# Optimization experiments

Measured on AMD Instinct MI355X. Metric: run time of the kernel, lower is better.

The kernel has to match this reference:

```python
import jax, jax.numpy as jnp
import numpy as np

D = 1024      # in_features
H = 768       # hidden_features per routed expert
E = 8         # n_routed_experts
K = 2         # n_activated_experts
NS = 2        # n_shared_experts
ROUTE_SCALE = 1.0


def setup_inputs() -> dict:
    key = jax.random.key(0)
    ks = jax.random.split(key, 6)
    s = 0.02
    return {
        "x": jax.random.normal(ks[0], (2, 1024, D), jnp.float32),
        "gate_w": jax.random.normal(ks[1], (E, D), jnp.float32) * s,
        "W1": jax.random.normal(ks[2], (E, 2 * H, D), jnp.float32) * s,   # expert fc1 (y|gate)
        "W2": jax.random.normal(ks[3], (E, D, H), jnp.float32) * s,       # expert fc2
        "Ws1": jax.random.normal(ks[4], (2 * NS * H, D), jnp.float32) * s,  # shared fc1
        "Ws2": jax.random.normal(ks[5], (D, NS * H), jnp.float32) * s,      # shared fc2
    }


def _gated_mlp(x, w1, w2):
    # GatedMLP: fc1 -> chunk(2) -> y * silu(gate) -> fc2, all bias-free
    h = x @ w1.T
    y, g = jnp.split(h, 2, axis=-1)
    return (y * jax.nn.silu(g)) @ w2.T


def reference(x, gate_w, W1, W2, Ws1, Ws2):
    x_shape = x.shape
    xf = x.reshape(-1, D)                 # [T, D]
    T = xf.shape[0]

    # --- Gate: softmax scores in fp32, top-k routing ---
    scores = jax.nn.softmax((xf @ gate_w.T).astype(jnp.float32), axis=-1)  # [T, E]
    top_vals, top_idx = jax.lax.top_k(scores, K)
    # no bias branch (in_features != 7168): gathered original scores == top_k values
    weights = (top_vals * ROUTE_SCALE).astype(x.dtype)                      # [T, K]

    # Dense per-token/expert combine weights (0 for unselected experts);
    # mathematically identical to the per-expert gather/scatter-add combine.
    w_dense = jnp.zeros((T, E), x.dtype).at[jnp.arange(T)[:, None], top_idx].set(weights)

    # --- Routed experts (stacked GatedMLPs) ---
    h = jnp.einsum('td,ehd->teh', xf, W1)        # [T, E, 2H]
    y, g = jnp.split(h, 2, axis=-1)
    eo = jnp.einsum('teh,edh->ted', y * jax.nn.silu(g), W2)  # [T, E, D]
    z = jnp.einsum('te,ted->td', w_dense, eo)    # weighted combine

    # --- Shared experts ---
    z = z + _gated_mlp(xf, Ws1, Ws2)
    return z.reshape(x_shape)
```

## Files before the change

### kernel.cpp

```cpp
#include <hip/hip_runtime.h>
#include <hip/hip_bf16.h>


typedef short bf16x8 __attribute__((ext_vector_type(8)));
typedef float f32x4 __attribute__((ext_vector_type(4)));

__device__ __forceinline__ unsigned short f2b(float f) {
    __hip_bfloat16 h = __float2bfloat16(f);
    return *reinterpret_cast<unsigned short*>(&h);
}

__device__ __forceinline__ void ldst16(const unsigned short* g, unsigned short* l) {
    __builtin_amdgcn_global_load_lds(
        (const __attribute__((address_space(1))) unsigned int*)g,
        (__attribute__((address_space(3))) unsigned int*)l, 16, 0, 0);
}

__device__ __forceinline__ void cvt8(const float* s, unsigned short* d, int j) {
    const float4* sp = reinterpret_cast<const float4*>(s) + (size_t)j * 2;
    float4 v0 = sp[0], v1 = sp[1];
    union { unsigned short u[8]; uint4 v; } o;
    o.u[0]=f2b(v0.x); o.u[1]=f2b(v0.y); o.u[2]=f2b(v0.z); o.u[3]=f2b(v0.w);
    o.u[4]=f2b(v1.x); o.u[5]=f2b(v1.y); o.u[6]=f2b(v1.z); o.u[7]=f2b(v1.w);
    *(reinterpret_cast<uint4*>(d) + j) = o.v;
}

__global__ __launch_bounds__(256) void k_convgate(const float* __restrict__ x,
                                                  const float* __restrict__ gw,
                                                  const float* __restrict__ W1,
                                                  const float* __restrict__ Ws1,
                                                  const float* __restrict__ W2,
                                                  const float* __restrict__ Ws2,
                                                  unsigned short* __restrict__ xb,
                                                  unsigned short* __restrict__ W1b,
                                                  unsigned short* __restrict__ Ws1b,
                                                  unsigned short* __restrict__ W2b,
                                                  unsigned short* __restrict__ Ws2b,
                                                  int* __restrict__ tokslot,
                                                  float* __restrict__ wroute,
                                                  int* __restrict__ cnt,
                                                  float* __restrict__ out) {
    __shared__ float red[4][8];
    __shared__ float sc[8];
    const int b = blockIdx.x, tid = threadIdx.x;
    if (b < 11520) {
        int i = b * 256 + tid;
        if (i < 1572864)       cvt8(W1,  W1b,  i);
        else if (i < 1966080)  cvt8(Ws1, Ws1b, i - 1572864);
        else if (i < 2752512)  cvt8(W2,  W2b,  i - 1966080);
        else if (i < 2949120)  cvt8(Ws2, Ws2b, i - 2752512);
        return;
    }
    const int t = b - 11520;
    const int lane = tid & 63, w = tid >> 6;

    float4 v = reinterpret_cast<const float4*>(x + (size_t)t * 1024)[tid];
    union { unsigned short u[4]; } o;
    o.u[0]=f2b(v.x); o.u[1]=f2b(v.y); o.u[2]=f2b(v.z); o.u[3]=f2b(v.w);
    reinterpret_cast<ushort4*>(xb + (size_t)t * 1024)[tid] = *(ushort4*)o.u;

    float p[8];
    for (int e = 0; e < 8; e++) {
        float4 g = reinterpret_cast<const float4*>(gw + (size_t)e * 1024)[tid];
        p[e] = v.x*g.x + v.y*g.y + v.z*g.z + v.w*g.w;
    }
    for (int e = 0; e < 8; e++)
        for (int off = 32; off > 0; off >>= 1) p[e] += __shfl_down(p[e], off, 64);
    if (lane == 0)
        for (int e = 0; e < 8; e++) red[w][e] = p[e];
    __syncthreads();
    if (tid < 8) sc[tid] = red[0][tid] + red[1][tid] + red[2][tid] + red[3][tid];
    __syncthreads();
    if (tid == 0) {
        float m = sc[0];
        for (int e = 1; e < 8; e++) m = fmaxf(m, sc[e]);
        float ex[8], sum = 0.f;
        for (int e = 0; e < 8; e++) { ex[e] = expf(sc[e] - m); sum += ex[e]; }
        float inv = 1.f / sum;
        int i1 = 0;
        for (int e = 1; e < 8; e++) if (sc[e] > sc[i1]) i1 = e;
        int i2 = -1; float s2 = -1e30f;
        for (int e = 0; e < 8; e++) if (e != i1 && sc[e] > s2) { s2 = sc[e]; i2 = e; }
        int p1 = atomicAdd(&cnt[i1 * 16], 1);
        tokslot[i1 * 2048 + p1] = t; wroute[i1 * 2048 + p1] = ex[i1] * inv;
        int p2 = atomicAdd(&cnt[i2 * 16], 1);
        tokslot[i2 * 2048 + p2] = t; wroute[i2 * 2048 + p2] = ex[i2] * inv;
    }
    reinterpret_cast<float4*>(out + (size_t)t * 1024)[tid] = (float4){0.f, 0.f, 0.f, 0.f};
}

__global__ __launch_bounds__(256) void k_fc1u(const unsigned short* __restrict__ xb,
                                              const unsigned short* __restrict__ W1b,
                                              const unsigned short* __restrict__ Ws1b,
                                              const int* __restrict__ tokslot,
                                              const float* __restrict__ wroute,
                                              const int* __restrict__ cnt,
                                              unsigned short* __restrict__ act_r,
                                              unsigned short* __restrict__ acts) {
    __shared__ alignas(16) unsigned short As[128 * 64];
    __shared__ alignas(16) unsigned short Bs[128 * 64];
    const int tid = threadIdx.x, lane = tid & 63, w = tid >> 6;
    const int wr = w >> 1, wc = w & 1;
    const int mt = blockIdx.x / 12, ht = blockIdx.x % 12;

    int pre = 0, sel = -1, base = 0;
    for (int ee = 0; ee < 10; ee++) {
        int til = (ee < 8) ? ((cnt[ee * 16] + 127) >> 7) : 16;
        if (sel < 0 && mt < pre + til) { sel = ee; base = pre; }
        pre += til;
    }
    if (sel < 0) return;
    const int e = sel, m0 = (mt - base) * 128, h0 = ht * 64;
    const int Te = (e < 8) ? cnt[e * 16] : 2048;
    const unsigned short* Bp = (e < 8) ? (W1b + (size_t)e * 1536 * 1024)
                                       : (Ws1b + (size_t)(e - 8) * 768 * 1024);
    const int gOff = (e < 8) ? 768 : 1536;

    const int kc = tid & 7;
    int aoff[4], boff[4];
    for (int q = 0; q < 4; q++) {
        int row = q * 32 + (tid >> 3);
        int idx = m0 + row;
        int tk = (e < 8) ? ((idx < Te) ? tokslot[e * 2048 + idx] : 0) : idx;
        aoff[q] = tk * 1024 + ((kc ^ (row & 7)) << 3);
        int grow = (row < 64) ? (h0 + row) : (gOff + h0 + row - 64);
        boff[q] = grow * 1024 + ((kc ^ (row & 7)) << 3);
    }

    f32x4 accy[4][2], accg[4][2];
    for (int i = 0; i < 4; i++)
        for (int j = 0; j < 2; j++) {
            accy[i][j] = (f32x4){0.f, 0.f, 0.f, 0.f};
            accg[i][j] = (f32x4){0.f, 0.f, 0.f, 0.f};
        }

    for (int k0 = 0; k0 < 1024; k0 += 64) {
        for (int q = 0; q < 4; q++) {
            ldst16(xb + aoff[q] + k0, As + (q * 256 + tid) * 8);
            ldst16(Bp + boff[q] + k0, Bs + (q * 256 + tid) * 8);
        }
        __syncthreads();
        for (int kh = 0; kh < 2; kh++) {
            const int cq = kh * 4 + (lane >> 4);
            bf16x8 a[4], by[2], bg[2];
            for (int i = 0; i < 4; i++) {
                int r = 64 * wr + 16 * i + (lane & 15);
                a[i] = *(const bf16x8*)&As[r * 64 + ((cq ^ (r & 7)) << 3)];
            }
            for (int j = 0; j < 2; j++) {
                int ry = 32 * wc + 16 * j + (lane & 15);
                by[j] = *(const bf16x8*)&Bs[ry * 64 + ((cq ^ (ry & 7)) << 3)];
                int rg = 64 + ry;
                bg[j] = *(const bf16x8*)&Bs[rg * 64 + ((cq ^ (rg & 7)) << 3)];
            }
            for (int i = 0; i < 4; i++)
                for (int j = 0; j < 2; j++) {
                    accy[i][j] = __builtin_amdgcn_mfma_f32_16x16x32_bf16(a[i], by[j], accy[i][j], 0, 0, 0);
                    accg[i][j] = __builtin_amdgcn_mfma_f32_16x16x32_bf16(a[i], bg[j], accg[i][j], 0, 0, 0);
                }
        }
        __syncthreads();
    }

    for (int i = 0; i < 4; i++)
        for (int r = 0; r < 4; r++) {
            int irow = m0 + 64 * wr + 16 * i + ((lane >> 4) << 2) + r;
            if (irow >= Te) continue;
            float sw = (e < 8) ? wroute[e * 2048 + irow] : 1.0f;
            unsigned short* dst = (e < 8)
                ? (act_r + ((size_t)e * 2048 + irow) * 768)
                : (acts + (size_t)irow * 1536 + (size_t)(e - 8) * 768);
            for (int j = 0; j < 2; j++) {
                float y = accy[i][j][r], g = accg[i][j][r];
                float sg = g / (1.0f + __expf(-g));
                int col = h0 + 32 * wc + 16 * j + (lane & 15);
                dst[col] = f2b(sw * y * sg);
            }
        }
}

__global__ __launch_bounds__(256) void k_fc2u(const unsigned short* __restrict__ act_r,
                                              const unsigned short* __restrict__ acts,
                                              const unsigned short* __restrict__ W2b,
                                              const unsigned short* __restrict__ Ws2b,
                                              const int* __restrict__ tokslot,
                                              const int* __restrict__ cnt,
                                              float* __restrict__ out) {
    __shared__ alignas(16) unsigned short As[128 * 128];
    __shared__ alignas(16) unsigned short Bs[64 * 128];
    const int tid = threadIdx.x, lane = tid & 63, w = tid >> 6;
    const int wr = w >> 1, wc = w & 1;
    const int mt = blockIdx.x >> 4, nt = blockIdx.x & 15;

    int pre = 0, sel = -1, base = 0;
    for (int ee = 0; ee < 9; ee++) {
        int til = (ee < 8) ? ((cnt[ee * 16] + 127) >> 7) : 16;
        if (sel < 0 && mt < pre + til) { sel = ee; base = pre; }
        pre += til;
    }
    if (sel < 0) return;
    const int e = sel, m0 = (mt - base) * 128, n0 = nt * 64;
    int Te, astride, bstride, K;
    const unsigned short *Ab, *Bb;
    if (e < 8) {
        Te = cnt[e * 16]; K = 768; astride = 768; bstride = 768;
        Ab = act_r + (size_t)e * 2048 * 768;
        Bb = W2b + (size_t)e * 1024 * 768;
    } else {
        Te = 2048; K = 1536; astride = 1536; bstride = 1536;
        Ab = acts;
        Bb = Ws2b;
    }

    const int cp = tid & 15;
    int aoff[8], boff[4];
    for (int q = 0; q < 8; q++) {
        int row = q * 16 + (tid >> 4);
        aoff[q] = (m0 + row) * astride + ((cp ^ (row & 15)) << 3);
    }
    for (int q = 0; q < 4; q++) {
        int row = q * 16 + (tid >> 4);
        boff[q] = (n0 + row) * bstride + ((cp ^ (row & 15)) << 3);
    }

    f32x4 acc[4][2];
    for (int i = 0; i < 4; i++)
        for (int j = 0; j < 2; j++) acc[i][j] = (f32x4){0.f, 0.f, 0.f, 0.f};

    for (int k0 = 0; k0 < K; k0 += 128) {
        for (int q = 0; q < 8; q++) ldst16(Ab + aoff[q] + k0, As + (q * 256 + tid) * 8);
        for (int q = 0; q < 4; q++) ldst16(Bb + boff[q] + k0, Bs + (q * 256 + tid) * 8);
        __syncthreads();
        for (int kh = 0; kh < 4; kh++) {
            const int cq = kh * 4 + (lane >> 4);
            bf16x8 a[4], b[2];
            for (int i = 0; i < 4; i++) {
                int r = 64 * wr + 16 * i + (lane & 15);
                a[i] = *(const bf16x8*)&As[r * 128 + ((cq ^ (r & 15)) << 3)];
            }
            for (int j = 0; j < 2; j++) {
                int rb = 32 * wc + 16 * j + (lane & 15);
                b[j] = *(const bf16x8*)&Bs[rb * 128 + ((cq ^ (rb & 15)) << 3)];
            }
            for (int i = 0; i < 4; i++)
                for (int j = 0; j < 2; j++)
                    acc[i][j] = __builtin_amdgcn_mfma_f32_16x16x32_bf16(a[i], b[j], acc[i][j], 0, 0, 0);
        }
        __syncthreads();
    }

    for (int i = 0; i < 4; i++)
        for (int r = 0; r < 4; r++) {
            int irow = m0 + 64 * wr + 16 * i + ((lane >> 4) << 2) + r;
            if (irow >= Te) continue;
            int t = (e < 8) ? tokslot[e * 2048 + irow] : irow;
            for (int j = 0; j < 2; j++) {
                int col = n0 + 32 * wc + 16 * j + (lane & 15);
                atomicAdd(out + (size_t)t * 1024 + col, acc[i][j][r]);
            }
        }
}

extern "C" void kernel_launch(void* const* d_in, const int* in_sizes, int n_in,
                              void* d_out, int out_size, void* d_ws, size_t ws_size,
                              hipStream_t stream) {
    const float* x   = (const float*)d_in[0];
    const float* gw  = (const float*)d_in[1];
    const float* W1  = (const float*)d_in[2];
    const float* W2  = (const float*)d_in[3];
    const float* Ws1 = (const float*)d_in[4];
    const float* Ws2 = (const float*)d_in[5];
    float* out = (float*)d_out;

    char* ws = (char*)d_ws;
    unsigned short* xb    = (unsigned short*)(ws + 0);
    unsigned short* W1b   = (unsigned short*)(ws + 4194304);
    unsigned short* Ws1b  = (unsigned short*)(ws + 29360128);
    unsigned short* W2b   = (unsigned short*)(ws + 35651584);
    unsigned short* Ws2b  = (unsigned short*)(ws + 48234496);
    unsigned short* act_r = (unsigned short*)(ws + 51380224);
    unsigned short* acts  = (unsigned short*)(ws + 76546048);
    int*            tokslot = (int*)(ws + 82837504);
    float*          wroute  = (float*)(ws + 82903040);
    int*            cnt     = (int*)(ws + 82968576);

    hipMemsetAsync(cnt, 0, 512, stream);
    k_convgate<<<13568, 256, 0, stream>>>(x, gw, W1, Ws1, W2, Ws2,
                                          xb, W1b, Ws1b, W2b, Ws2b,
                                          tokslot, wroute, cnt, out);
    k_fc1u<<<864, 256, 0, stream>>>(xb, W1b, Ws1b, tokslot, wroute, cnt, act_r, acts);
    k_fc2u<<<896, 256, 0, stream>>>(act_r, acts, W2b, Ws2b, tokslot, cnt, out);
}
```

Baseline: 236.3 us.

## Double-buffer LDS tiles in fc1/fc2 GEMMs to overlap loads with MFMA

Both expert GEMM kernels now keep two LDS buffers and issue the global-to-LDS loads for the next K slice before running the MFMAs on the current one, with a single waitcnt and barrier per iteration. The fc2 kernel's K tile is cut from 128 to 64 so the doubled buffers fit in LDS, and s_setprio is raised around the MFMA blocks. The aim is to hide global-memory latency behind compute. The cost is more LDS per block in fc1, which can lower occupancy, and twice as many loop iterations and barriers in fc2.

```diff
diff --git a/kernel.cpp b/kernel.cpp
--- a/kernel.cpp
+++ b/kernel.cpp
@@ -97,8 +97,8 @@
                                               const int* __restrict__ cnt,
                                               unsigned short* __restrict__ act_r,
                                               unsigned short* __restrict__ acts) {
-    __shared__ alignas(16) unsigned short As[128 * 64];
-    __shared__ alignas(16) unsigned short Bs[128 * 64];
+    __shared__ alignas(16) unsigned short As[2][128 * 64];
+    __shared__ alignas(16) unsigned short Bs[2][128 * 64];
     const int tid = threadIdx.x, lane = tid & 63, w = tid >> 6;
     const int wr = w >> 1, wc = w & 1;
     const int mt = blockIdx.x / 12, ht = blockIdx.x % 12;
@@ -134,32 +134,44 @@
             accg[i][j] = (f32x4){0.f, 0.f, 0.f, 0.f};
         }
 
+    auto stage = [&](int buf, int k0) {
+        for (int q = 0; q < 4; q++) {
+            ldst16(xb + aoff[q] + k0, &As[buf][(q * 256 + tid) * 8]);
+            ldst16(Bp + boff[q] + k0, &Bs[buf][(q * 256 + tid) * 8]);
+        }
+    };
+
+    stage(0, 0);
+    asm volatile("s_waitcnt vmcnt(0)" ::: "memory");
+    __builtin_amdgcn_s_barrier();
+
+    int cur = 0;
     for (int k0 = 0; k0 < 1024; k0 += 64) {
-        for (int q = 0; q < 4; q++) {
-            ldst16(xb + aoff[q] + k0, As + (q * 256 + tid) * 8);
-            ldst16(Bp + boff[q] + k0, Bs + (q * 256 + tid) * 8);
-        }
-        __syncthreads();
+        if (k0 + 64 < 1024) stage(cur ^ 1, k0 + 64);
         for (int kh = 0; kh < 2; kh++) {
             const int cq = kh * 4 + (lane >> 4);
             bf16x8 a[4], by[2], bg[2];
             for (int i = 0; i < 4; i++) {
                 int r = 64 * wr + 16 * i + (lane & 15);
-                a[i] = *(const bf16x8*)&As[r * 64 + ((cq ^ (r & 7)) << 3)];
+                a[i] = *(const bf16x8*)&As[cur][r * 64 + ((cq ^ (r & 7)) << 3)];
             }
             for (int j = 0; j < 2; j++) {
                 int ry = 32 * wc + 16 * j + (lane & 15);
-                by[j] = *(const bf16x8*)&Bs[ry * 64 + ((cq ^ (ry & 7)) << 3)];
+                by[j] = *(const bf16x8*)&Bs[cur][ry * 64 + ((cq ^ (ry & 7)) << 3)];
                 int rg = 64 + ry;
-                bg[j] = *(const bf16x8*)&Bs[rg * 64 + ((cq ^ (rg & 7)) << 3)];
-            }
+                bg[j] = *(const bf16x8*)&Bs[cur][rg * 64 + ((cq ^ (rg & 7)) << 3)];
+            }
+            __builtin_amdgcn_s_setprio(1);
             for (int i = 0; i < 4; i++)
                 for (int j = 0; j < 2; j++) {
                     accy[i][j] = __builtin_amdgcn_mfma_f32_16x16x32_bf16(a[i], by[j], accy[i][j], 0, 0, 0);
                     accg[i][j] = __builtin_amdgcn_mfma_f32_16x16x32_bf16(a[i], bg[j], accg[i][j], 0, 0, 0);
                 }
-        }
-        __syncthreads();
+            __builtin_amdgcn_s_setprio(0);
+        }
+        asm volatile("s_waitcnt vmcnt(0)" ::: "memory");
+        __builtin_amdgcn_s_barrier();
+        cur ^= 1;
     }
 
     for (int i = 0; i < 4; i++)
@@ -186,8 +198,8 @@
                                               const int* __restrict__ tokslot,
                                               const int* __restrict__ cnt,
                                               float* __restrict__ out) {
-    __shared__ alignas(16) unsigned short As[128 * 128];
-    __shared__ alignas(16) unsigned short Bs[64 * 128];
+    __shared__ alignas(16) unsigned short As[2][128 * 64];
+    __shared__ alignas(16) unsigned short Bs[2][64 * 64];
     const int tid = threadIdx.x, lane = tid & 63, w = tid >> 6;
     const int wr = w >> 1, wc = w & 1;
     const int mt = blockIdx.x >> 4, nt = blockIdx.x & 15;
@@ -212,41 +224,53 @@
         Bb = Ws2b;
     }
 
-    const int cp = tid & 15;
-    int aoff[8], boff[4];
-    for (int q = 0; q < 8; q++) {
-        int row = q * 16 + (tid >> 4);
-        aoff[q] = (m0 + row) * astride + ((cp ^ (row & 15)) << 3);
-    }
+    const int kc = tid & 7;
+    int aoff[4], boff[2];
     for (int q = 0; q < 4; q++) {
-        int row = q * 16 + (tid >> 4);
-        boff[q] = (n0 + row) * bstride + ((cp ^ (row & 15)) << 3);
+        int row = q * 32 + (tid >> 3);
+        aoff[q] = (m0 + row) * astride + ((kc ^ (row & 7)) << 3);
+    }
+    for (int q = 0; q < 2; q++) {
+        int row = q * 32 + (tid >> 3);
+        boff[q] = (n0 + row) * bstride + ((kc ^ (row & 7)) << 3);
     }
 
     f32x4 acc[4][2];
     for (int i = 0; i < 4; i++)
         for (int j = 0; j < 2; j++) acc[i][j] = (f32x4){0.f, 0.f, 0.f, 0.f};
 
-    for (int k0 = 0; k0 < K; k0 += 128) {
-        for (int q = 0; q < 8; q++) ldst16(Ab + aoff[q] + k0, As + (q * 256 + tid) * 8);
-        for (int q = 0; q < 4; q++) ldst16(Bb + boff[q] + k0, Bs + (q * 256 + tid) * 8);
-        __syncthreads();
-        for (int kh = 0; kh < 4; kh++) {
+    auto stage = [&](int buf, int k0) {
+        for (int q = 0; q < 4; q++) ldst16(Ab + aoff[q] + k0, &As[buf][(q * 256 + tid) * 8]);
+        for (int q = 0; q < 2; q++) ldst16(Bb + boff[q] + k0, &Bs[buf][(q * 256 + tid) * 8]);
+    };
+
+    stage(0, 0);
+    asm volatile("s_waitcnt vmcnt(0)" ::: "memory");
+    __builtin_amdgcn_s_barrier();
+
+    int cur = 0;
+    for (int k0 = 0; k0 < K; k0 += 64) {
+        if (k0 + 64 < K) stage(cur ^ 1, k0 + 64);
+        for (int kh = 0; kh < 2; kh++) {
             const int cq = kh * 4 + (lane >> 4);
             bf16x8 a[4], b[2];
             for (int i = 0; i < 4; i++) {
                 int r = 64 * wr + 16 * i + (lane & 15);
-                a[i] = *(const bf16x8*)&As[r * 128 + ((cq ^ (r & 15)) << 3)];
+                a[i] = *(const bf16x8*)&As[cur][r * 64 + ((cq ^ (r & 7)) << 3)];
             }
             for (int j = 0; j < 2; j++) {
                 int rb = 32 * wc + 16 * j + (lane & 15);
-                b[j] = *(const bf16x8*)&Bs[rb * 128 + ((cq ^ (rb & 15)) << 3)];
-            }
+                b[j] = *(const bf16x8*)&Bs[cur][rb * 64 + ((cq ^ (rb & 7)) << 3)];
+            }
+            __builtin_amdgcn_s_setprio(1);
             for (int i = 0; i < 4; i++)
                 for (int j = 0; j < 2; j++)
                     acc[i][j] = __builtin_amdgcn_mfma_f32_16x16x32_bf16(a[i], b[j], acc[i][j], 0, 0, 0);
-        }
-        __syncthreads();
+            __builtin_amdgcn_s_setprio(0);
+        }
+        asm volatile("s_waitcnt vmcnt(0)" ::: "memory");
+        __builtin_amdgcn_s_barrier();
+        cur ^= 1;
     }
 
     for (int i = 0; i < 4; i++)
```

New measurement: 235.6 us. About the same (-0.3%).

## Fuse MoE stages into one persistent cooperative kernel with work queues

Applied to the files above, without the earlier changes.

Replaces the three kernel launches with one persistent cooperative kernel that uses grid-wide syncs between phases. Blocks take work from atomic counters. The W2/Ws2 fp32-to-bf16 conversion is deferred into the fc1 phase so it overlaps with the fc1 GEMM tiles, and fc2 tiles are handed out in reverse order. It also raises wave priority around the MFMA blocks. The aim is to cut launch gaps and tail idle time, at the cost of grid-sync overhead and occupancy fixed by the persistent grid size.

```diff
diff --git a/kernel.cpp b/kernel.cpp
--- a/kernel.cpp
+++ b/kernel.cpp
@@ -1,5 +1,8 @@
 #include <hip/hip_runtime.h>
 #include <hip/hip_bf16.h>
+#include <hip/hip_cooperative_groups.h>
+
+namespace cg = cooperative_groups;
 
 
 typedef short bf16x8 __attribute__((ext_vector_type(8)));
@@ -25,83 +28,21 @@
     *(reinterpret_cast<uint4*>(d) + j) = o.v;
 }
 
-__global__ __launch_bounds__(256) void k_convgate(const float* __restrict__ x,
-                                                  const float* __restrict__ gw,
-                                                  const float* __restrict__ W1,
-                                                  const float* __restrict__ Ws1,
-                                                  const float* __restrict__ W2,
-                                                  const float* __restrict__ Ws2,
-                                                  unsigned short* __restrict__ xb,
-                                                  unsigned short* __restrict__ W1b,
-                                                  unsigned short* __restrict__ Ws1b,
-                                                  unsigned short* __restrict__ W2b,
-                                                  unsigned short* __restrict__ Ws2b,
-                                                  int* __restrict__ tokslot,
-                                                  float* __restrict__ wroute,
-                                                  int* __restrict__ cnt,
-                                                  float* __restrict__ out) {
-    __shared__ float red[4][8];
-    __shared__ float sc[8];
-    const int b = blockIdx.x, tid = threadIdx.x;
-    if (b < 11520) {
-        int i = b * 256 + tid;
-        if (i < 1572864)       cvt8(W1,  W1b,  i);
-        else if (i < 1966080)  cvt8(Ws1, Ws1b, i - 1572864);
-        else if (i < 2752512)  cvt8(W2,  W2b,  i - 1966080);
-        else if (i < 2949120)  cvt8(Ws2, Ws2b, i - 2752512);
-        return;
-    }
-    const int t = b - 11520;
-    const int lane = tid & 63, w = tid >> 6;
-
-    float4 v = reinterpret_cast<const float4*>(x + (size_t)t * 1024)[tid];
-    union { unsigned short u[4]; } o;
-    o.u[0]=f2b(v.x); o.u[1]=f2b(v.y); o.u[2]=f2b(v.z); o.u[3]=f2b(v.w);
-    reinterpret_cast<ushort4*>(xb + (size_t)t * 1024)[tid] = *(ushort4*)o.u;
-
-    float p[8];
-    for (int e = 0; e < 8; e++) {
-        float4 g = reinterpret_cast<const float4*>(gw + (size_t)e * 1024)[tid];
-        p[e] = v.x*g.x + v.y*g.y + v.z*g.z + v.w*g.w;
-    }
-    for (int e = 0; e < 8; e++)
-        for (int off = 32; off > 0; off >>= 1) p[e] += __shfl_down(p[e], off, 64);
-    if (lane == 0)
-        for (int e = 0; e < 8; e++) red[w][e] = p[e];
-    __syncthreads();
-    if (tid < 8) sc[tid] = red[0][tid] + red[1][tid] + red[2][tid] + red[3][tid];
-    __syncthreads();
-    if (tid == 0) {
-        float m = sc[0];
-        for (int e = 1; e < 8; e++) m = fmaxf(m, sc[e]);
-        float ex[8], sum = 0.f;
-        for (int e = 0; e < 8; e++) { ex[e] = expf(sc[e] - m); sum += ex[e]; }
-        float inv = 1.f / sum;
-        int i1 = 0;
-        for (int e = 1; e < 8; e++) if (sc[e] > sc[i1]) i1 = e;
-        int i2 = -1; float s2 = -1e30f;
-        for (int e = 0; e < 8; e++) if (e != i1 && sc[e] > s2) { s2 = sc[e]; i2 = e; }
-        int p1 = atomicAdd(&cnt[i1 * 16], 1);
-        tokslot[i1 * 2048 + p1] = t; wroute[i1 * 2048 + p1] = ex[i1] * inv;
-        int p2 = atomicAdd(&cnt[i2 * 16], 1);
-        tokslot[i2 * 2048 + p2] = t; wroute[i2 * 2048 + p2] = ex[i2] * inv;
-    }
-    reinterpret_cast<float4*>(out + (size_t)t * 1024)[tid] = (float4){0.f, 0.f, 0.f, 0.f};
-}
-
-__global__ __launch_bounds__(256) void k_fc1u(const unsigned short* __restrict__ xb,
-                                              const unsigned short* __restrict__ W1b,
-                                              const unsigned short* __restrict__ Ws1b,
-                                              const int* __restrict__ tokslot,
-                                              const float* __restrict__ wroute,
-                                              const int* __restrict__ cnt,
-                                              unsigned short* __restrict__ act_r,
-                                              unsigned short* __restrict__ acts) {
-    __shared__ alignas(16) unsigned short As[128 * 64];
-    __shared__ alignas(16) unsigned short Bs[128 * 64];
+__device__ void fc1_tile(int tile, unsigned short* smem,
+                         const unsigned short* __restrict__ xb,
+                         const unsigned short* __restrict__ W1b,
+                         const unsigned short* __restrict__ Ws1b,
+                         const int* __restrict__ tokslot,
+                         const float* __restrict__ wroute,
+                         const int* __restrict__ cnt,
+                         unsigned short* __restrict__ act_r,
+                         unsigned short* __restrict__ acts)
+{
+    unsigned short* As = smem;
+    unsigned short* Bs = smem + 8192;
     const int tid = threadIdx.x, lane = tid & 63, w = tid >> 6;
     const int wr = w >> 1, wc = w & 1;
-    const int mt = blockIdx.x / 12, ht = blockIdx.x % 12;
+    const int mt = tile / 12, ht = tile % 12;
 
     int pre = 0, sel = -1, base = 0;
     for (int ee = 0; ee < 10; ee++) {
@@ -153,11 +94,13 @@
                 int rg = 64 + ry;
                 bg[j] = *(const bf16x8*)&Bs[rg * 64 + ((cq ^ (rg & 7)) << 3)];
             }
+            __builtin_amdgcn_s_setprio(1);
             for (int i = 0; i < 4; i++)
                 for (int j = 0; j < 2; j++) {
                     accy[i][j] = __builtin_amdgcn_mfma_f32_16x16x32_bf16(a[i], by[j], accy[i][j], 0, 0, 0);
                     accg[i][j] = __builtin_amdgcn_mfma_f32_16x16x32_bf16(a[i], bg[j], accg[i][j], 0, 0, 0);
                 }
+            __builtin_amdgcn_s_setprio(0);
         }
         __syncthreads();
     }
@@ -179,18 +122,20 @@
         }
 }
 
-__global__ __launch_bounds__(256) void k_fc2u(const unsigned short* __restrict__ act_r,
-                                              const unsigned short* __restrict__ acts,
-                                              const unsigned short* __restrict__ W2b,
-                                              const unsigned short* __restrict__ Ws2b,
-                                              const int* __restrict__ tokslot,
-                                              const int* __restrict__ cnt,
-                                              float* __restrict__ out) {
-    __shared__ alignas(16) unsigned short As[128 * 128];
-    __shared__ alignas(16) unsigned short Bs[64 * 128];
+__device__ void fc2_tile(int tile, unsigned short* smem,
+                         const unsigned short* __restrict__ act_r,
+                         const unsigned short* __restrict__ acts,
+                         const unsigned short* __restrict__ W2b,
+                         const unsigned short* __restrict__ Ws2b,
+                         const int* __restrict__ tokslot,
+                         const int* __restrict__ cnt,
+                         float* __restrict__ out)
+{
+    unsigned short* As = smem;
+    unsigned short* Bs = smem + 16384;
     const int tid = threadIdx.x, lane = tid & 63, w = tid >> 6;
     const int wr = w >> 1, wc = w & 1;
-    const int mt = blockIdx.x >> 4, nt = blockIdx.x & 15;
+    const int mt = tile >> 4, nt = tile & 15;
 
     int pre = 0, sel = -1, base = 0;
     for (int ee = 0; ee < 9; ee++) {
@@ -242,9 +187,11 @@
                 int rb = 32 * wc + 16 * j + (lane & 15);
                 b[j] = *(const bf16x8*)&Bs[rb * 128 + ((cq ^ (rb & 15)) << 3)];
             }
+            __builtin_amdgcn_s_setprio(1);
             for (int i = 0; i < 4; i++)
                 for (int j = 0; j < 2; j++)
                     acc[i][j] = __builtin_amdgcn_mfma_f32_16x16x32_bf16(a[i], b[j], acc[i][j], 0, 0, 0);
+            __builtin_amdgcn_s_setprio(0);
         }
         __syncthreads();
     }
@@ -259,6 +206,107 @@
                 atomicAdd(out + (size_t)t * 1024 + col, acc[i][j][r]);
             }
         }
+}
+
+__global__ __launch_bounds__(256, 3) void k_moe(
+    const float* __restrict__ x, const float* __restrict__ gw,
+    const float* __restrict__ W1, const float* __restrict__ Ws1,
+    const float* __restrict__ W2, const float* __restrict__ Ws2,
+    unsigned short* __restrict__ xb, unsigned short* __restrict__ W1b,
+    unsigned short* __restrict__ Ws1b, unsigned short* __restrict__ W2b,
+    unsigned short* __restrict__ Ws2b, int* __restrict__ tokslot,
+    float* __restrict__ wroute, int* __restrict__ cnt,
+    unsigned short* __restrict__ act_r, unsigned short* __restrict__ acts,
+    float* __restrict__ out)
+{
+    __shared__ alignas(16) unsigned short smem[24576];
+    const int tid = threadIdx.x, bid = blockIdx.x, nb = gridDim.x;
+    cg::grid_group grid = cg::this_grid();
+
+    {
+        const int stride = nb * 256;
+        for (int i = bid * 256 + tid; i < 1966080; i += stride) {
+            if (i < 1572864) cvt8(W1, W1b, i);
+            else             cvt8(Ws1, Ws1b, i - 1572864);
+        }
+        const int lane = tid & 63, w = tid >> 6;
+        float* red = (float*)smem;
+        float* sc  = red + 32;
+        for (int t = bid; t < 2048; t += nb) {
+            float4 v = reinterpret_cast<const float4*>(x + (size_t)t * 1024)[tid];
+            union { unsigned short u[4]; ushort4 v4; } o;
+            o.u[0]=f2b(v.x); o.u[1]=f2b(v.y); o.u[2]=f2b(v.z); o.u[3]=f2b(v.w);
+            reinterpret_cast<ushort4*>(xb + (size_t)t * 1024)[tid] = o.v4;
+
+            float p[8];
+            for (int e = 0; e < 8; e++) {
+                float4 g = reinterpret_cast<const float4*>(gw + (size_t)e * 1024)[tid];
+                p[e] = v.x*g.x + v.y*g.y + v.z*g.z + v.w*g.w;
+            }
+            for (int e = 0; e < 8; e++)
+                for (int off = 32; off > 0; off >>= 1) p[e] += __shfl_down(p[e], off, 64);
+            if (lane == 0)
+                for (int e = 0; e < 8; e++) red[w * 8 + e] = p[e];
+            __syncthreads();
+            if (tid < 8) sc[tid] = red[tid] + red[8 + tid] + red[16 + tid] + red[24 + tid];
+            __syncthreads();
+            if (tid == 0) {
+                float m = sc[0];
+                for (int e = 1; e < 8; e++) m = fmaxf(m, sc[e]);
+                float ex[8], sum = 0.f;
+                for (int e = 0; e < 8; e++) { ex[e] = expf(sc[e] - m); sum += ex[e]; }
+                float inv = 1.f / sum;
+                int i1 = 0;
+                for (int e = 1; e < 8; e++) if (sc[e] > sc[i1]) i1 = e;
+                int i2 = -1; float s2 = -1e30f;
+                for (int e = 0; e < 8; e++) if (e != i1 && sc[e] > s2) { s2 = sc[e]; i2 = e; }
+                int p1 = atomicAdd(&cnt[i1 * 16], 1);
+                tokslot[i1 * 2048 + p1] = t; wroute[i1 * 2048 + p1] = ex[i1] * inv;
+                int p2 = atomicAdd(&cnt[i2 * 16], 1);
+                tokslot[i2 * 2048 + p2] = t; wroute[i2 * 2048 + p2] = ex[i2] * inv;
+            }
+            reinterpret_cast<float4*>(out + (size_t)t * 1024)[tid] = (float4){0.f, 0.f, 0.f, 0.f};
+            __syncthreads();
+        }
+    }
+    __threadfence();
+    grid.sync();
+
+    {
+        int* bc = (int*)smem;
+        while (true) {
+            if (tid == 0) *bc = atomicAdd(cnt + 120, 1);
+            __syncthreads();
+            const int item = *bc;
+            __syncthreads();
+            if (item >= 1824) break;
+            if (item < 864) {
+                fc1_tile(item, smem, xb, W1b, Ws1b, tokslot, wroute, cnt, act_r, acts);
+            } else {
+                const int c0 = (item - 864) * 1024 + tid;
+                #pragma unroll
+                for (int u = 0; u < 4; u++) {
+                    int i = c0 + u * 256;
+                    if (i < 786432)       cvt8(W2, W2b, i);
+                    else                  cvt8(Ws2, Ws2b, i - 786432);
+                }
+            }
+        }
+    }
+    __threadfence();
+    grid.sync();
+
+    {
+        int* bc = (int*)smem;
+        while (true) {
+            if (tid == 0) *bc = atomicAdd(cnt + 124, 1);
+            __syncthreads();
+            const int item = *bc;
+            __syncthreads();
+            if (item >= 896) break;
+            fc2_tile(895 - item, smem, act_r, acts, W2b, Ws2b, tokslot, cnt, out);
+        }
+    }
 }
 
 extern "C" void kernel_launch(void* const* d_in, const int* in_sizes, int n_in,
@@ -284,10 +332,19 @@
     float*          wroute  = (float*)(ws + 82903040);
     int*            cnt     = (int*)(ws + 82968576);
 
+    static int gridsz = 0;
+    if (gridsz == 0) {
+        int nbpc = 0;
+        if (hipOccupancyMaxActiveBlocksPerMultiprocessor(&nbpc, k_moe, 256, 0) != hipSuccess
+            || nbpc < 1) nbpc = 1;
+        if (nbpc > 3) nbpc = 3;
+        gridsz = nbpc * 256;
+    }
+
     hipMemsetAsync(cnt, 0, 512, stream);
-    k_convgate<<<13568, 256, 0, stream>>>(x, gw, W1, Ws1, W2, Ws2,
-                                          xb, W1b, Ws1b, W2b, Ws2b,
-                                          tokslot, wroute, cnt, out);
-    k_fc1u<<<864, 256, 0, stream>>>(xb, W1b, Ws1b, tokslot, wroute, cnt, act_r, acts);
-    k_fc2u<<<896, 256, 0, stream>>>(act_r, acts, W2b, Ws2b, tokslot, cnt, out);
-}
+    void* args[] = {(void*)&x, (void*)&gw, (void*)&W1, (void*)&Ws1, (void*)&W2, (void*)&Ws2,
+                    (void*)&xb, (void*)&W1b, (void*)&Ws1b, (void*)&W2b, (void*)&Ws2b,
+                    (void*)&tokslot, (void*)&wroute, (void*)&cnt,
+                    (void*)&act_r, (void*)&acts, (void*)&out};
+    hipLaunchCooperativeKernel((void*)k_moe, dim3(gridsz), dim3(256), args, 0, stream);
+}
```

Result: slower. 443.5 us (+87.7%).

## Remap GEMM block indices per XCD and double per-thread weight conversion work

Applied to the files above, without the earlier changes.

The fc1 and fc2 kernels now decode blockIdx so that the blocks landing on one XCD (blockIdx mod 8) share the same M-tiles and sweep all N/H tiles of each. The aim is to reuse the gathered activation rows from that XCD's L2 instead of spreading them across all eight XCDs. The weight-conversion part of k_convgate now has each thread convert two 8-element chunks, which halves the number of conversion blocks and cuts per-block scheduling overhead. Nothing changes numerically. Because the routed expert tile counts are uneven, the remap may leave work unevenly spread across XCDs.

```diff
diff --git a/kernel.cpp b/kernel.cpp
--- a/kernel.cpp
+++ b/kernel.cpp
@@ -23,6 +23,17 @@
     o.u[0]=f2b(v0.x); o.u[1]=f2b(v0.y); o.u[2]=f2b(v0.z); o.u[3]=f2b(v0.w);
     o.u[4]=f2b(v1.x); o.u[5]=f2b(v1.y); o.u[6]=f2b(v1.z); o.u[7]=f2b(v1.w);
     *(reinterpret_cast<uint4*>(d) + j) = o.v;
+}
+
+__device__ __forceinline__ void cvt_dispatch(const float* W1, const float* Ws1,
+                                             const float* W2, const float* Ws2,
+                                             unsigned short* W1b, unsigned short* Ws1b,
+                                             unsigned short* W2b, unsigned short* Ws2b,
+                                             int i) {
+    if (i < 1572864)       cvt8(W1,  W1b,  i);
+    else if (i < 1966080)  cvt8(Ws1, Ws1b, i - 1572864);
+    else if (i < 2752512)  cvt8(W2,  W2b,  i - 1966080);
+    else if (i < 2949120)  cvt8(Ws2, Ws2b, i - 2752512);
 }
 
 __global__ __launch_bounds__(256) void k_convgate(const float* __restrict__ x,
@@ -43,15 +54,13 @@
     __shared__ float red[4][8];
     __shared__ float sc[8];
     const int b = blockIdx.x, tid = threadIdx.x;
-    if (b < 11520) {
-        int i = b * 256 + tid;
-        if (i < 1572864)       cvt8(W1,  W1b,  i);
-        else if (i < 1966080)  cvt8(Ws1, Ws1b, i - 1572864);
-        else if (i < 2752512)  cvt8(W2,  W2b,  i - 1966080);
-        else if (i < 2949120)  cvt8(Ws2, Ws2b, i - 2752512);
+    if (b < 5760) {
+        int i0 = b * 512 + tid;
+        cvt_dispatch(W1, Ws1, W2, Ws2, W1b, Ws1b, W2b, Ws2b, i0);
+        cvt_dispatch(W1, Ws1, W2, Ws2, W1b, Ws1b, W2b, Ws2b, i0 + 256);
         return;
     }
-    const int t = b - 11520;
+    const int t = b - 5760;
     const int lane = tid & 63, w = tid >> 6;
 
     float4 v = reinterpret_cast<const float4*>(x + (size_t)t * 1024)[tid];
@@ -101,7 +110,8 @@
     __shared__ alignas(16) unsigned short Bs[128 * 64];
     const int tid = threadIdx.x, lane = tid & 63, w = tid >> 6;
     const int wr = w >> 1, wc = w & 1;
-    const int mt = blockIdx.x / 12, ht = blockIdx.x % 12;
+    const int xcd = blockIdx.x & 7, j = blockIdx.x >> 3;
+    const int mt = (j / 12) * 8 + xcd, ht = j % 12;
 
     int pre = 0, sel = -1, base = 0;
     for (int ee = 0; ee < 10; ee++) {
@@ -129,9 +139,9 @@
 
     f32x4 accy[4][2], accg[4][2];
     for (int i = 0; i < 4; i++)
-        for (int j = 0; j < 2; j++) {
-            accy[i][j] = (f32x4){0.f, 0.f, 0.f, 0.f};
-            accg[i][j] = (f32x4){0.f, 0.f, 0.f, 0.f};
+        for (int j2 = 0; j2 < 2; j2++) {
+            accy[i][j2] = (f32x4){0.f, 0.f, 0.f, 0.f};
+            accg[i][j2] = (f32x4){0.f, 0.f, 0.f, 0.f};
         }
 
     for (int k0 = 0; k0 < 1024; k0 += 64) {
@@ -147,16 +157,16 @@
                 int r = 64 * wr + 16 * i + (lane & 15);
                 a[i] = *(const bf16x8*)&As[r * 64 + ((cq ^ (r & 7)) << 3)];
             }
-            for (int j = 0; j < 2; j++) {
-                int ry = 32 * wc + 16 * j + (lane & 15);
-                by[j] = *(const bf16x8*)&Bs[ry * 64 + ((cq ^ (ry & 7)) << 3)];
+            for (int j2 = 0; j2 < 2; j2++) {
+                int ry = 32 * wc + 16 * j2 + (lane & 15);
+                by[j2] = *(const bf16x8*)&Bs[ry * 64 + ((cq ^ (ry & 7)) << 3)];
                 int rg = 64 + ry;
-                bg[j] = *(const bf16x8*)&Bs[rg * 64 + ((cq ^ (rg & 7)) << 3)];
+                bg[j2] = *(const bf16x8*)&Bs[rg * 64 + ((cq ^ (rg & 7)) << 3)];
             }
             for (int i = 0; i < 4; i++)
-                for (int j = 0; j < 2; j++) {
-                    accy[i][j] = __builtin_amdgcn_mfma_f32_16x16x32_bf16(a[i], by[j], accy[i][j], 0, 0, 0);
-                    accg[i][j] = __builtin_amdgcn_mfma_f32_16x16x32_bf16(a[i], bg[j], accg[i][j], 0, 0, 0);
+                for (int j2 = 0; j2 < 2; j2++) {
+                    accy[i][j2] = __builtin_amdgcn_mfma_f32_16x16x32_bf16(a[i], by[j2], accy[i][j2], 0, 0, 0);
+                    accg[i][j2] = __builtin_amdgcn_mfma_f32_16x16x32_bf16(a[i], bg[j2], accg[i][j2], 0, 0, 0);
                 }
         }
         __syncthreads();
@@ -170,10 +180,10 @@
             unsigned short* dst = (e < 8)
                 ? (act_r + ((size_t)e * 2048 + irow) * 768)
                 : (acts + (size_t)irow * 1536 + (size_t)(e - 8) * 768);
-            for (int j = 0; j < 2; j++) {
-                float y = accy[i][j][r], g = accg[i][j][r];
+            for (int j2 = 0; j2 < 2; j2++) {
+                float y = accy[i][j2][r], g = accg[i][j2][r];
                 float sg = g / (1.0f + __expf(-g));
-                int col = h0 + 32 * wc + 16 * j + (lane & 15);
+                int col = h0 + 32 * wc + 16 * j2 + (lane & 15);
                 dst[col] = f2b(sw * y * sg);
             }
         }
@@ -190,7 +200,8 @@
     __shared__ alignas(16) unsigned short Bs[64 * 128];
     const int tid = threadIdx.x, lane = tid & 63, w = tid >> 6;
     const int wr = w >> 1, wc = w & 1;
-    const int mt = blockIdx.x >> 4, nt = blockIdx.x & 15;
+    const int xcd = blockIdx.x & 7, j = blockIdx.x >> 3;
+    const int mt = (j / 16) * 8 + xcd, nt = j % 16;
 
     int pre = 0, sel = -1, base = 0;
     for (int ee = 0; ee < 9; ee++) {
@@ -225,7 +236,7 @@
 
     f32x4 acc[4][2];
     for (int i = 0; i < 4; i++)
-        for (int j = 0; j < 2; j++) acc[i][j] = (f32x4){0.f, 0.f, 0.f, 0.f};
+        for (int j2 = 0; j2 < 2; j2++) acc[i][j2] = (f32x4){0.f, 0.f, 0.f, 0.f};
 
     for (int k0 = 0; k0 < K; k0 += 128) {
         for (int q = 0; q < 8; q++) ldst16(Ab + aoff[q] + k0, As + (q * 256 + tid) * 8);
@@ -238,13 +249,13 @@
                 int r = 64 * wr + 16 * i + (lane & 15);
                 a[i] = *(const bf16x8*)&As[r * 128 + ((cq ^ (r & 15)) << 3)];
             }
-            for (int j = 0; j < 2; j++) {
-                int rb = 32 * wc + 16 * j + (lane & 15);
-                b[j] = *(const bf16x8*)&Bs[rb * 128 + ((cq ^ (rb & 15)) << 3)];
+            for (int j2 = 0; j2 < 2; j2++) {
+                int rb = 32 * wc + 16 * j2 + (lane & 15);
+                b[j2] = *(const bf16x8*)&Bs[rb * 128 + ((cq ^ (rb & 15)) << 3)];
             }
             for (int i = 0; i < 4; i++)
-                for (int j = 0; j < 2; j++)
-                    acc[i][j] = __builtin_amdgcn_mfma_f32_16x16x32_bf16(a[i], b[j], acc[i][j], 0, 0, 0);
+                for (int j2 = 0; j2 < 2; j2++)
+                    acc[i][j2] = __builtin_amdgcn_mfma_f32_16x16x32_bf16(a[i], b[j2], acc[i][j2], 0, 0, 0);
         }
         __syncthreads();
     }
@@ -254,9 +265,9 @@
             int irow = m0 + 64 * wr + 16 * i + ((lane >> 4) << 2) + r;
             if (irow >= Te) continue;
             int t = (e < 8) ? tokslot[e * 2048 + irow] : irow;
-            for (int j = 0; j < 2; j++) {
-                int col = n0 + 32 * wc + 16 * j + (lane & 15);
-                atomicAdd(out + (size_t)t * 1024 + col, acc[i][j][r]);
+            for (int j2 = 0; j2 < 2; j2++) {
+                int col = n0 + 32 * wc + 16 * j2 + (lane & 15);
+                atomicAdd(out + (size_t)t * 1024 + col, acc[i][j2][r]);
             }
         }
 }
@@ -285,9 +296,9 @@
     int*            cnt     = (int*)(ws + 82968576);
 
     hipMemsetAsync(cnt, 0, 512, stream);
-    k_convgate<<<13568, 256, 0, stream>>>(x, gw, W1, Ws1, W2, Ws2,
-                                          xb, W1b, Ws1b, W2b, Ws2b,
-                                          tokslot, wroute, cnt, out);
+    k_convgate<<<7808, 256, 0, stream>>>(x, gw, W1, Ws1, W2, Ws2,
+                                         xb, W1b, Ws1b, W2b, Ws2b,
+                                         tokslot, wroute, cnt, out);
     k_fc1u<<<864, 256, 0, stream>>>(xb, W1b, Ws1b, tokslot, wroute, cnt, act_r, acts);
     k_fc2u<<<896, 256, 0, stream>>>(act_r, acts, W2b, Ws2b, tokslot, cnt, out);
 }
```

After: 244.0 us. +3.3%, slower.
